# Optimization experiments

Measured on AMD Instinct MI355X. Metric: run time of the kernel, lower is better.

The kernel has to match this reference:

```python
import jax, jax.numpy as jnp
import numpy as np

D_MODEL, Q, V, H = 1024, 64, 64, 16
B, K = 2, 2048


def setup_inputs() -> dict:
    key = jax.random.key(0)
    ks = jax.random.split(key, 8)
    s = 0.02
    return {
        "xi": jax.random.normal(ks[0], (B, K, D_MODEL), dtype=jnp.float32),
        # stacked per-head projection weights (equivalent to h separate nn.Linear)
        "Wq": jax.random.normal(ks[1], (H, D_MODEL, Q), dtype=jnp.float32) * s,
        "bq": jax.random.normal(ks[2], (H, Q), dtype=jnp.float32) * s,
        "Wk": jax.random.normal(ks[3], (H, D_MODEL, Q), dtype=jnp.float32) * s,
        "bk": jax.random.normal(ks[4], (H, Q), dtype=jnp.float32) * s,
        "Wv": jax.random.normal(ks[5], (H, D_MODEL, V), dtype=jnp.float32) * s,
        "bv": jax.random.normal(ks[6], (H, V), dtype=jnp.float32) * s,
        "Wo": jax.random.normal(ks[7], (H * V, D_MODEL), dtype=jnp.float32) * s,
        "bo": jnp.zeros((D_MODEL,), dtype=jnp.float32),
    }


def reference(xi, Wq, bq, Wk, bk, Wv, bv, Wo, bo):
    # per-head projections, batched over heads: [B,H,K,q]
    queries = jnp.einsum("bkd,hdq->bhkq", xi, Wq) + bq[None, :, None, :]
    keys = jnp.einsum("bkd,hdq->bhkq", xi, Wk) + bk[None, :, None, :]
    values = jnp.einsum("bkd,hdv->bhkv", xi, Wv) + bv[None, :, None, :]
    # NOTE: original scales by sqrt(queries.shape[1]) == sqrt(seq_len K), not sqrt(q)
    scale = 1.0 / np.sqrt(xi.shape[1]).astype(np.float32)
    scores = jax.nn.softmax(jnp.einsum("bhkq,bhmq->bhkm", queries, keys) * scale, axis=-1)
    attn = jnp.einsum("bhkm,bhmv->bhkv", scores, values)  # [B,H,K,v]
    # concat heads along last dim -> [B,K,H*v]
    attn = attn.transpose(0, 2, 1, 3).reshape(xi.shape[0], xi.shape[1], -1)
    return attn @ Wo + bo
```

## Files before the change

### kernel.cpp

```cpp
#include <hip/hip_runtime.h>
#include <math.h>

typedef __bf16 bf16x8 __attribute__((ext_vector_type(8)));
typedef float  f32x4  __attribute__((ext_vector_type(4)));
typedef float  f32x16 __attribute__((ext_vector_type(16)));
typedef unsigned short u16x8 __attribute__((ext_vector_type(8)));

#define D_MODEL 1024
#define QDIM    64
#define HEADS   16
#define BATCH   2
#define SEQ     2048
#define M_ROWS  (BATCH*SEQ)
#define NCAT    (HEADS*3*QDIM)

__device__ __forceinline__ unsigned short f2bf(float f) {
    unsigned int u = __float_as_uint(f);
    u += 0x7fffu + ((u >> 16) & 1u);
    return (unsigned short)(u >> 16);
}

__device__ __forceinline__ void gl16(const unsigned short* g, unsigned short* l) {
    __builtin_amdgcn_global_load_lds(
        (const __attribute__((address_space(1))) unsigned int*)g,
        (__attribute__((address_space(3))) unsigned int*)l, 16, 0, 0);
}

__global__ __launch_bounds__(256) void k_cvt_bf16(const float* __restrict__ in,
                                                  unsigned short* __restrict__ out) {
    int i = (blockIdx.x * 256 + threadIdx.x) * 8;
    f32x4 a = *(const f32x4*)(in + i);
    f32x4 b = *(const f32x4*)(in + i + 4);
    u16x8 o;
    o[0]=f2bf(a[0]); o[1]=f2bf(a[1]); o[2]=f2bf(a[2]); o[3]=f2bf(a[3]);
    o[4]=f2bf(b[0]); o[5]=f2bf(b[1]); o[6]=f2bf(b[2]); o[7]=f2bf(b[3]);
    *(u16x8*)(out + i) = o;
}

__global__ __launch_bounds__(256) void k_prep_wcat(const float* __restrict__ Wq,
                                                   const float* __restrict__ Wk,
                                                   const float* __restrict__ Wv,
                                                   const float* __restrict__ bq,
                                                   const float* __restrict__ bk,
                                                   const float* __restrict__ bv,
                                                   unsigned short* __restrict__ WcatT,
                                                   float* __restrict__ bcat,
                                                   float qscale) {
    int blk = blockIdx.x;
    int dt = blk & 15, h = (blk >> 4) & 15, s = blk >> 8;
    const float* W = (s == 0) ? Wq : (s == 1) ? Wk : Wv;
    float sc = (s == 0) ? qscale : 1.0f;
    __shared__ float t[64][65];
    int tid = threadIdx.x;
    int dr = tid >> 2, qc = (tid & 3) * 16;
    const float* src = W + (size_t)h * (D_MODEL * QDIM) + (size_t)(dt * 64 + dr) * QDIM + qc;
#pragma unroll
    for (int j = 0; j < 4; ++j) {
        f32x4 v = *(const f32x4*)(src + j * 4);
        t[dr][qc + j * 4 + 0] = v[0]; t[dr][qc + j * 4 + 1] = v[1];
        t[dr][qc + j * 4 + 2] = v[2]; t[dr][qc + j * 4 + 3] = v[3];
    }
    __syncthreads();
    int q = tid >> 2, dc = (tid & 3) * 16;
    unsigned short* dst = WcatT + (size_t)(h * 192 + s * 64 + q) * D_MODEL + dt * 64 + dc;
#pragma unroll
    for (int j = 0; j < 2; ++j) {
        u16x8 o;
#pragma unroll
        for (int e = 0; e < 8; ++e) o[e] = f2bf(t[dc + j * 8 + e][q] * sc);
        *(u16x8*)(dst + j * 8) = o;
    }
    if (dt == 0 && tid < 64) {
        const float* bb = (s == 0) ? bq : (s == 1) ? bk : bv;
        bcat[h * 192 + s * 64 + tid] = bb[h * QDIM + tid] * sc;
    }
}

__global__ __launch_bounds__(256) void k_prep_wo(const float* __restrict__ Wo,
                                                 unsigned short* __restrict__ WoT) {
    int blk = blockIdx.x;
    int ct = blk & 15, rt = blk >> 4;
    __shared__ float t[64][65];
    int tid = threadIdx.x;
    int dr = tid >> 2, qc = (tid & 3) * 16;
    const float* src = Wo + (size_t)(rt * 64 + dr) * D_MODEL + ct * 64 + qc;
#pragma unroll
    for (int j = 0; j < 4; ++j) {
        f32x4 v = *(const f32x4*)(src + j * 4);
        t[dr][qc + j * 4 + 0] = v[0]; t[dr][qc + j * 4 + 1] = v[1];
        t[dr][qc + j * 4 + 2] = v[2]; t[dr][qc + j * 4 + 3] = v[3];
    }
    __syncthreads();
    int q = tid >> 2, dc = (tid & 3) * 16;
    unsigned short* dst = WoT + (size_t)(ct * 64 + q) * D_MODEL + rt * 64 + dc;
#pragma unroll
    for (int j = 0; j < 2; ++j) {
        u16x8 o;
#pragma unroll
        for (int e = 0; e < 8; ++e) o[e] = f2bf(t[dc + j * 8 + e][q]);
        *(u16x8*)(dst + j * 8) = o;
    }
}

template<bool OUT_BF16>
__global__ __launch_bounds__(256) void k_gemm(const unsigned short* __restrict__ A,
                                              const unsigned short* __restrict__ BT,
                                              const float* __restrict__ bias,
                                              void* __restrict__ Cout,
                                              int N, int Kd) {
    __shared__ __align__(16) unsigned char smem[65536];
    const int tid = threadIdx.x;
    const int lane = tid & 63, w = tid >> 6;
    const int g = lane >> 4, c = lane & 15;
    int nwg = gridDim.x * gridDim.y;
    int bid = blockIdx.y * gridDim.x + blockIdx.x;
    int sw = (bid & 7) * (nwg >> 3) + (bid >> 3);
    int bx = sw % gridDim.x, by = sw / gridDim.x;
    const int m0 = by * 128, n0 = bx * 128;
    const int wm = (w >> 1) * 64, wn = (w & 1) * 64;
    f32x4 acc[4][4] = {};

    const int srow = w * 16 + (lane >> 2);
    const int scol = ((lane & 3) ^ ((lane >> 3) & 3)) * 8;
    const unsigned short* pA0 = A  + (size_t)(m0 + srow) * Kd + scol;
    const unsigned short* pA1 = pA0 + (size_t)64 * Kd;
    const unsigned short* pB0 = BT + (size_t)(n0 + srow) * Kd + scol;
    const unsigned short* pB1 = pB0 + (size_t)64 * Kd;
    const int kc = (c >> 1) & 3;
    const int aoff = (wm + c) * 64 + ((g ^ kc) * 16);
    const int boff = (wn + c) * 64 + ((g ^ kc) * 16);

#define STAGE(buf)                                                                   \
    {                                                                                \
        unsigned short* lb = (unsigned short*)(smem + (buf) * 16384) + w * 512;      \
        gl16(pA0, lb);                                                               \
        gl16(pA1, lb + 2048);                                                        \
        gl16(pB0, lb + 4096);                                                        \
        gl16(pB1, lb + 6144);                                                        \
        pA0 += 32; pA1 += 32; pB0 += 32; pB1 += 32;                                  \
    }

#define COMPUTE(buf)                                                                 \
    {                                                                                \
        const unsigned char* Ab = smem + (buf) * 16384;                              \
        const unsigned char* Bb = Ab + 8192;                                         \
        bf16x8 af[4], bfr[4];                                                        \
        _Pragma("unroll") for (int mf = 0; mf < 4; ++mf)                             \
            af[mf] = *(const bf16x8*)(Ab + mf * 1024 + aoff);                        \
        _Pragma("unroll") for (int nf = 0; nf < 4; ++nf)                             \
            bfr[nf] = *(const bf16x8*)(Bb + nf * 1024 + boff);                       \
        __builtin_amdgcn_s_setprio(1);                                               \
        _Pragma("unroll") for (int mf = 0; mf < 4; ++mf)                             \
            _Pragma("unroll") for (int nf = 0; nf < 4; ++nf)                         \
                acc[mf][nf] = __builtin_amdgcn_mfma_f32_16x16x32_bf16(               \
                    af[mf], bfr[nf], acc[mf][nf], 0, 0, 0);                          \
        __builtin_amdgcn_s_setprio(0);                                               \
    }

    const int nt = Kd >> 5;
    STAGE(0); STAGE(1); STAGE(2);

    for (int t = 0; t < nt - 3; ++t) {
        STAGE((t + 3) & 3);
        asm volatile("s_waitcnt vmcnt(12)" ::: "memory");
        __builtin_amdgcn_s_barrier();
        __builtin_amdgcn_sched_barrier(0);
        COMPUTE(t & 3);
        __builtin_amdgcn_sched_barrier(0);
        __builtin_amdgcn_s_barrier();
    }
    asm volatile("s_waitcnt vmcnt(8)" ::: "memory");
    __builtin_amdgcn_s_barrier();
    __builtin_amdgcn_sched_barrier(0);
    COMPUTE((nt - 3) & 3);
    __builtin_amdgcn_sched_barrier(0);
    __builtin_amdgcn_s_barrier();
    asm volatile("s_waitcnt vmcnt(4)" ::: "memory");
    __builtin_amdgcn_s_barrier();
    __builtin_amdgcn_sched_barrier(0);
    COMPUTE((nt - 2) & 3);
    __builtin_amdgcn_sched_barrier(0);
    __builtin_amdgcn_s_barrier();
    asm volatile("s_waitcnt vmcnt(0)" ::: "memory");
    __builtin_amdgcn_s_barrier();
    __builtin_amdgcn_sched_barrier(0);
    COMPUTE((nt - 1) & 3);
#undef STAGE
#undef COMPUTE

#pragma unroll
    for (int mf = 0; mf < 4; ++mf)
#pragma unroll
        for (int nf = 0; nf < 4; ++nf) {
            int col = n0 + wn + nf * 16 + c;
            float bb = bias[col];
#pragma unroll
            for (int r = 0; r < 4; ++r) {
                int row = m0 + wm + mf * 16 + 4 * g + r;
                float v = acc[mf][nf][r] + bb;
                if (OUT_BF16)
                    ((unsigned short*)Cout)[(size_t)row * N + col] = f2bf(v);
                else
                    ((float*)Cout)[(size_t)row * N + col] = v;
            }
        }
}

__global__ __launch_bounds__(256) void k_repack(const unsigned short* __restrict__ qkv,
                                                unsigned short* __restrict__ kfrag,
                                                unsigned short* __restrict__ vfrag) {
    int blk = blockIdx.x;
    int kt = blk & 31, h = (blk >> 5) & 15, b = blk >> 9;
    __shared__ unsigned short ktile[64][72];
    __shared__ unsigned short vtile[64][72];
    int tid = threadIdx.x;
#pragma unroll
    for (int j = 0; j < 2; ++j) {
        int cid = tid + j * 256;
        int row = cid >> 3, ch = (cid & 7) * 8;
        const unsigned short* base = qkv + (size_t)(b * SEQ + kt * 64 + row) * NCAT + h * 192;
        *(u16x8*)&ktile[row][ch] = *(const u16x8*)(base + 64 + ch);
        *(u16x8*)&vtile[row][ch] = *(const u16x8*)(base + 128 + ch);
    }
    __syncthreads();
    size_t obase = (size_t)blk * 4096;
#pragma unroll
    for (int j = 0; j < 2; ++j) {
        int p = tid + j * 256;
        int f = p >> 6, l31 = p & 31, hi = (p >> 5) & 1;
        *(u16x8*)(kfrag + obase + p * 8) =
            *(const u16x8*)&ktile[(f >> 2) * 32 + l31][(f & 3) * 16 + hi * 8];
        int vv = (f & 1) * 32 + l31;
        int k0 = (f >> 2) * 32 + ((f >> 1) & 1) * 16 + hi * 8;
        u16x8 o;
#pragma unroll
        for (int e = 0; e < 8; ++e) o[e] = vtile[k0 + e][vv];
        *(u16x8*)(vfrag + obase + p * 8) = o;
    }
}

__global__ __launch_bounds__(256) void k_attn(const unsigned short* __restrict__ qkv,
                                              const unsigned short* __restrict__ kfrag,
                                              const unsigned short* __restrict__ vfrag,
                                              unsigned short* __restrict__ attn) {
    int bid = blockIdx.x;
    int blk = (bid & 7) * 128 + (bid >> 3);
    int qt = blk & 31, h = (blk >> 5) & 15, b = blk >> 9;
    int tid = threadIdx.x, w = tid >> 6, lane = tid & 63;
    int l31 = lane & 31, hi = lane >> 5;
    int qh = w & 1, kh = w >> 1;

    __shared__ __align__(16) unsigned char KV[2][16384];

    const int qbase = b * SEQ + qt * 64;
    const unsigned short* qrow = qkv + (size_t)(qbase + qh * 32 + l31) * NCAT + h * 192;
    bf16x8 qf[4];
#pragma unroll
    for (int s = 0; s < 4; ++s) qf[s] = *(const bf16x8*)(qrow + s * 16 + hi * 8);

    f32x16 o0 = {}, o1 = {};
    float rsum = 0.f;

    const size_t fb = (size_t)(b * 512 + h * 32) * 4096;
    const unsigned short* ks0 = kfrag + fb + (w)     * 512 + lane * 8;
    const unsigned short* ks1 = kfrag + fb + (w + 4) * 512 + lane * 8;
    const unsigned short* vs0 = vfrag + fb + (w)     * 512 + lane * 8;
    const unsigned short* vs1 = vfrag + fb + (w + 4) * 512 + lane * 8;
    const unsigned kd0 = w * 1024, kd1 = (w + 4) * 1024;
    const unsigned vd0 = 8192 + w * 1024, vd1 = 8192 + (w + 4) * 1024;
    const int lx = lane * 16;

    gl16(ks0, (unsigned short*)&KV[0][kd0]);
    gl16(vs0, (unsigned short*)&KV[0][vd0]);
    gl16(ks1, (unsigned short*)&KV[0][kd1]);
    gl16(vs1, (unsigned short*)&KV[0][vd1]);
    ks0 += 4096; ks1 += 4096; vs0 += 4096; vs1 += 4096;
    asm volatile("s_waitcnt vmcnt(0)" ::: "memory");
    __builtin_amdgcn_s_barrier();

    const int NT = SEQ / 64;
    for (int t = 0; t < NT; ++t) {
        const int cur = t & 1;
        if (t + 1 < NT) {
            gl16(ks0, (unsigned short*)&KV[cur ^ 1][kd0]);
            gl16(vs0, (unsigned short*)&KV[cur ^ 1][vd0]);
            gl16(ks1, (unsigned short*)&KV[cur ^ 1][kd1]);
            gl16(vs1, (unsigned short*)&KV[cur ^ 1][vd1]);
            ks0 += 4096; ks1 += 4096; vs0 += 4096; vs1 += 4096;
            asm volatile("s_waitcnt vmcnt(4)" ::: "memory");
        } else {
            asm volatile("s_waitcnt vmcnt(0)" ::: "memory");
        }
        __builtin_amdgcn_s_barrier();
        __builtin_amdgcn_sched_barrier(0);

        const unsigned char* Kf = &KV[cur][0];
        const unsigned char* Vf = &KV[cur][8192];

        f32x16 st = {};
        __builtin_amdgcn_s_setprio(1);
#pragma unroll
        for (int s = 0; s < 4; ++s) {
            bf16x8 kf = *(const bf16x8*)(Kf + (kh * 4 + s) * 1024 + lx);
            st = __builtin_amdgcn_mfma_f32_32x32x16_bf16(kf, qf[s], st, 0, 0, 0);
        }
        __builtin_amdgcn_s_setprio(0);

#pragma unroll
        for (int r = 0; r < 16; ++r) {
            float p = __builtin_amdgcn_exp2f(st[r]);
            st[r] = p;
            rsum += p;
        }
        unsigned int d0, d1, d2, d3, d4, d5, d6, d7;
        asm("v_cvt_pk_bf16_f32 %0, %1, %2" : "=v"(d0) : "v"(st[0]),  "v"(st[1]));
        asm("v_cvt_pk_bf16_f32 %0, %1, %2" : "=v"(d1) : "v"(st[2]),  "v"(st[3]));
        asm("v_cvt_pk_bf16_f32 %0, %1, %2" : "=v"(d2) : "v"(st[4]),  "v"(st[5]));
        asm("v_cvt_pk_bf16_f32 %0, %1, %2" : "=v"(d3) : "v"(st[6]),  "v"(st[7]));
        asm("v_cvt_pk_bf16_f32 %0, %1, %2" : "=v"(d4) : "v"(st[8]),  "v"(st[9]));
        asm("v_cvt_pk_bf16_f32 %0, %1, %2" : "=v"(d5) : "v"(st[10]), "v"(st[11]));
        asm("v_cvt_pk_bf16_f32 %0, %1, %2" : "=v"(d6) : "v"(st[12]), "v"(st[13]));
        asm("v_cvt_pk_bf16_f32 %0, %1, %2" : "=v"(d7) : "v"(st[14]), "v"(st[15]));
        asm("v_permlane32_swap_b32 %0, %1" : "+v"(d0), "+v"(d2));
        asm("v_permlane32_swap_b32 %0, %1" : "+v"(d1), "+v"(d3));
        asm("v_permlane32_swap_b32 %0, %1" : "+v"(d4), "+v"(d6));
        asm("v_permlane32_swap_b32 %0, %1" : "+v"(d5), "+v"(d7));
        union { unsigned int u[4]; bf16x8 v; } pa0, pa1;
        pa0.u[0] = d0; pa0.u[1] = d1; pa0.u[2] = d2; pa0.u[3] = d3;
        pa1.u[0] = d4; pa1.u[1] = d5; pa1.u[2] = d6; pa1.u[3] = d7;

        __builtin_amdgcn_s_setprio(1);
        {
            bf16x8 vf00 = *(const bf16x8*)(Vf + (kh * 4 + 0) * 1024 + lx);
            bf16x8 vf01 = *(const bf16x8*)(Vf + (kh * 4 + 1) * 1024 + lx);
            bf16x8 vf10 = *(const bf16x8*)(Vf + (kh * 4 + 2) * 1024 + lx);
            bf16x8 vf11 = *(const bf16x8*)(Vf + (kh * 4 + 3) * 1024 + lx);
            o0 = __builtin_amdgcn_mfma_f32_32x32x16_bf16(pa0.v, vf00, o0, 0, 0, 0);
            o1 = __builtin_amdgcn_mfma_f32_32x32x16_bf16(pa0.v, vf01, o1, 0, 0, 0);
            o0 = __builtin_amdgcn_mfma_f32_32x32x16_bf16(pa1.v, vf10, o0, 0, 0, 0);
            o1 = __builtin_amdgcn_mfma_f32_32x32x16_bf16(pa1.v, vf11, o1, 0, 0, 0);
        }
        __builtin_amdgcn_s_setprio(0);
        __builtin_amdgcn_sched_barrier(0);
        __builtin_amdgcn_s_barrier();
    }

    rsum += __shfl_xor(rsum, 32);
    __syncthreads();
    float* red = (float*)&KV[0][0];
    float* rsb = (float*)&KV[1][0];
    if (kh == 1) {
#pragma unroll
        for (int r = 0; r < 16; ++r) {
            int q = (r & 3) + 8 * (r >> 2) + 4 * hi;
            red[(qh * 32 + q) * 64 + l31]      = o0[r];
            red[(qh * 32 + q) * 64 + 32 + l31] = o1[r];
        }
    }
    if (lane < 32) rsb[(kh * 2 + qh) * 32 + l31] = rsum;
    __syncthreads();
    if (kh == 0) {
#pragma unroll
        for (int r = 0; r < 16; ++r) {
            int q = (r & 3) + 8 * (r >> 2) + 4 * hi;
            float tot = rsb[qh * 32 + q] + rsb[(2 + qh) * 32 + q];
            float inv = 1.0f / tot;
            float v0 = (o0[r] + red[(qh * 32 + q) * 64 + l31]) * inv;
            float v1 = (o1[r] + red[(qh * 32 + q) * 64 + 32 + l31]) * inv;
            int row = qbase + qh * 32 + q;
            attn[(size_t)row * (HEADS * QDIM) + h * QDIM + l31]      = f2bf(v0);
            attn[(size_t)row * (HEADS * QDIM) + h * QDIM + 32 + l31] = f2bf(v1);
        }
    }
}

extern "C" void kernel_launch(void* const* d_in, const int* in_sizes, int n_in,
                              void* d_out, int out_size, void* d_ws, size_t ws_size,
                              hipStream_t stream) {
    const float* xi = (const float*)d_in[0];
    const float* Wq = (const float*)d_in[1];
    const float* bq = (const float*)d_in[2];
    const float* Wk = (const float*)d_in[3];
    const float* bk = (const float*)d_in[4];
    const float* Wv = (const float*)d_in[5];
    const float* bv = (const float*)d_in[6];
    const float* Wo = (const float*)d_in[7];
    const float* bo = (const float*)d_in[8];

    unsigned short* xi_bf = (unsigned short*)d_ws;
    unsigned short* WcatT = xi_bf + (size_t)M_ROWS * D_MODEL;
    unsigned short* WoT   = WcatT + (size_t)NCAT * D_MODEL;
    float*          bcat  = (float*)(WoT + (size_t)D_MODEL * D_MODEL);
    unsigned short* qkvc  = (unsigned short*)(bcat + NCAT);
    unsigned short* kfrag = qkvc + (size_t)M_ROWS * NCAT;
    unsigned short* vfrag = kfrag + (size_t)BATCH * HEADS * 32 * 4096;
    unsigned short* attnb = vfrag + (size_t)BATCH * HEADS * 32 * 4096;

    float qscale = 1.4426950408889634f / sqrtf((float)SEQ);

    k_cvt_bf16<<<(M_ROWS * D_MODEL) / 2048, 256, 0, stream>>>(xi, xi_bf);
    k_prep_wcat<<<768, 256, 0, stream>>>(Wq, Wk, Wv, bq, bk, bv, WcatT, bcat, qscale);
    k_prep_wo<<<256, 256, 0, stream>>>(Wo, WoT);

    k_gemm<true><<<dim3(NCAT / 128, M_ROWS / 128), 256, 0, stream>>>(
        xi_bf, WcatT, bcat, (void*)qkvc, NCAT, D_MODEL);

    k_repack<<<BATCH * HEADS * (SEQ / 64), 256, 0, stream>>>(qkvc, kfrag, vfrag);

    k_attn<<<BATCH * HEADS * (SEQ / 64), 256, 0, stream>>>(qkvc, kfrag, vfrag, attnb);

    k_gemm<false><<<dim3(D_MODEL / 128, M_ROWS / 128), 256, 0, stream>>>(
        attnb, WoT, bo, d_out, D_MODEL, D_MODEL);
}
```

Measured before the change: 127.1 us.

## Load K/V fragments directly to registers in attention and merge weight-prep kernels

The attention kernel drops the LDS double buffer and its barriers. Each wave now loads only the K/V fragments it uses (its kh half) straight from global memory into registers, ping-ponging between two register sets so the next tile's loads overlap the current tile's compute. This removes per-tile block synchronisation and LDS round trips, at the cost of more VGPRs and of relying on L2 hits, since the two waves sharing a kh read the same data. Separately, the Wqkv and Wo weight-transpose kernels are fused into one launch to save a kernel launch.

Measured after the change: 119.6 us. -5.9%, faster.

```diff
diff --git a/kernel.cpp b/kernel.cpp
--- a/kernel.cpp
+++ b/kernel.cpp
@@ -37,68 +37,66 @@
     *(u16x8*)(out + i) = o;
 }
 
-__global__ __launch_bounds__(256) void k_prep_wcat(const float* __restrict__ Wq,
-                                                   const float* __restrict__ Wk,
-                                                   const float* __restrict__ Wv,
-                                                   const float* __restrict__ bq,
-                                                   const float* __restrict__ bk,
-                                                   const float* __restrict__ bv,
-                                                   unsigned short* __restrict__ WcatT,
-                                                   float* __restrict__ bcat,
-                                                   float qscale) {
-    int blk = blockIdx.x;
-    int dt = blk & 15, h = (blk >> 4) & 15, s = blk >> 8;
-    const float* W = (s == 0) ? Wq : (s == 1) ? Wk : Wv;
-    float sc = (s == 0) ? qscale : 1.0f;
+__global__ __launch_bounds__(256) void k_prep_w(const float* __restrict__ Wq,
+                                                const float* __restrict__ Wk,
+                                                const float* __restrict__ Wv,
+                                                const float* __restrict__ bq,
+                                                const float* __restrict__ bk,
+                                                const float* __restrict__ bv,
+                                                const float* __restrict__ Wo,
+                                                unsigned short* __restrict__ WcatT,
+                                                float* __restrict__ bcat,
+                                                unsigned short* __restrict__ WoT,
+                                                float qscale) {
     __shared__ float t[64][65];
     int tid = threadIdx.x;
     int dr = tid >> 2, qc = (tid & 3) * 16;
-    const float* src = W + (size_t)h * (D_MODEL * QDIM) + (size_t)(dt * 64 + dr) * QDIM + qc;
-#pragma unroll
-    for (int j = 0; j < 4; ++j) {
-        f32x4 v = *(const f32x4*)(src + j * 4);
-        t[dr][qc + j * 4 + 0] = v[0]; t[dr][qc + j * 4 + 1] = v[1];
-        t[dr][qc + j * 4 + 2] = v[2]; t[dr][qc + j * 4 + 3] = v[3];
-    }
-    __syncthreads();
-    int q = tid >> 2, dc = (tid & 3) * 16;
-    unsigned short* dst = WcatT + (size_t)(h * 192 + s * 64 + q) * D_MODEL + dt * 64 + dc;
-#pragma unroll
-    for (int j = 0; j < 2; ++j) {
-        u16x8 o;
-#pragma unroll
-        for (int e = 0; e < 8; ++e) o[e] = f2bf(t[dc + j * 8 + e][q] * sc);
-        *(u16x8*)(dst + j * 8) = o;
-    }
-    if (dt == 0 && tid < 64) {
-        const float* bb = (s == 0) ? bq : (s == 1) ? bk : bv;
-        bcat[h * 192 + s * 64 + tid] = bb[h * QDIM + tid] * sc;
-    }
-}
-
-__global__ __launch_bounds__(256) void k_prep_wo(const float* __restrict__ Wo,
-                                                 unsigned short* __restrict__ WoT) {
-    int blk = blockIdx.x;
-    int ct = blk & 15, rt = blk >> 4;
-    __shared__ float t[64][65];
-    int tid = threadIdx.x;
-    int dr = tid >> 2, qc = (tid & 3) * 16;
-    const float* src = Wo + (size_t)(rt * 64 + dr) * D_MODEL + ct * 64 + qc;
-#pragma unroll
-    for (int j = 0; j < 4; ++j) {
-        f32x4 v = *(const f32x4*)(src + j * 4);
-        t[dr][qc + j * 4 + 0] = v[0]; t[dr][qc + j * 4 + 1] = v[1];
-        t[dr][qc + j * 4 + 2] = v[2]; t[dr][qc + j * 4 + 3] = v[3];
-    }
-    __syncthreads();
-    int q = tid >> 2, dc = (tid & 3) * 16;
-    unsigned short* dst = WoT + (size_t)(ct * 64 + q) * D_MODEL + rt * 64 + dc;
-#pragma unroll
-    for (int j = 0; j < 2; ++j) {
-        u16x8 o;
-#pragma unroll
-        for (int e = 0; e < 8; ++e) o[e] = f2bf(t[dc + j * 8 + e][q]);
-        *(u16x8*)(dst + j * 8) = o;
+    if (blockIdx.x < 768) {
+        int blk = blockIdx.x;
+        int dt = blk & 15, h = (blk >> 4) & 15, s = blk >> 8;
+        const float* W = (s == 0) ? Wq : (s == 1) ? Wk : Wv;
+        float sc = (s == 0) ? qscale : 1.0f;
+        const float* src = W + (size_t)h * (D_MODEL * QDIM) + (size_t)(dt * 64 + dr) * QDIM + qc;
+#pragma unroll
+        for (int j = 0; j < 4; ++j) {
+            f32x4 v = *(const f32x4*)(src + j * 4);
+            t[dr][qc + j * 4 + 0] = v[0]; t[dr][qc + j * 4 + 1] = v[1];
+            t[dr][qc + j * 4 + 2] = v[2]; t[dr][qc + j * 4 + 3] = v[3];
+        }
+        __syncthreads();
+        int q = tid >> 2, dc = (tid & 3) * 16;
+        unsigned short* dst = WcatT + (size_t)(h * 192 + s * 64 + q) * D_MODEL + dt * 64 + dc;
+#pragma unroll
+        for (int j = 0; j < 2; ++j) {
+            u16x8 o;
+#pragma unroll
+            for (int e = 0; e < 8; ++e) o[e] = f2bf(t[dc + j * 8 + e][q] * sc);
+            *(u16x8*)(dst + j * 8) = o;
+        }
+        if (dt == 0 && tid < 64) {
+            const float* bb = (s == 0) ? bq : (s == 1) ? bk : bv;
+            bcat[h * 192 + s * 64 + tid] = bb[h * QDIM + tid] * sc;
+        }
+    } else {
+        int blk = blockIdx.x - 768;
+        int ct = blk & 15, rt = blk >> 4;
+        const float* src = Wo + (size_t)(rt * 64 + dr) * D_MODEL + ct * 64 + qc;
+#pragma unroll
+        for (int j = 0; j < 4; ++j) {
+            f32x4 v = *(const f32x4*)(src + j * 4);
+            t[dr][qc + j * 4 + 0] = v[0]; t[dr][qc + j * 4 + 1] = v[1];
+            t[dr][qc + j * 4 + 2] = v[2]; t[dr][qc + j * 4 + 3] = v[3];
+        }
+        __syncthreads();
+        int q = tid >> 2, dc = (tid & 3) * 16;
+        unsigned short* dst = WoT + (size_t)(ct * 64 + q) * D_MODEL + rt * 64 + dc;
+#pragma unroll
+        for (int j = 0; j < 2; ++j) {
+            u16x8 o;
+#pragma unroll
+            for (int e = 0; e < 8; ++e) o[e] = f2bf(t[dc + j * 8 + e][q]);
+            *(u16x8*)(dst + j * 8) = o;
+        }
     }
 }
 
@@ -250,105 +248,87 @@
     int l31 = lane & 31, hi = lane >> 5;
     int qh = w & 1, kh = w >> 1;
 
-    __shared__ __align__(16) unsigned char KV[2][16384];
+    __shared__ float red[4096];
+    __shared__ float rsb[128];
 
     const int qbase = b * SEQ + qt * 64;
     const unsigned short* qrow = qkv + (size_t)(qbase + qh * 32 + l31) * NCAT + h * 192;
-    bf16x8 qf[4];
-#pragma unroll
-    for (int s = 0; s < 4; ++s) qf[s] = *(const bf16x8*)(qrow + s * 16 + hi * 8);
+    bf16x8 qf0 = *(const bf16x8*)(qrow + 0 * 16 + hi * 8);
+    bf16x8 qf1 = *(const bf16x8*)(qrow + 1 * 16 + hi * 8);
+    bf16x8 qf2 = *(const bf16x8*)(qrow + 2 * 16 + hi * 8);
+    bf16x8 qf3 = *(const bf16x8*)(qrow + 3 * 16 + hi * 8);
 
     f32x16 o0 = {}, o1 = {};
     float rsum = 0.f;
 
-    const size_t fb = (size_t)(b * 512 + h * 32) * 4096;
-    const unsigned short* ks0 = kfrag + fb + (w)     * 512 + lane * 8;
-    const unsigned short* ks1 = kfrag + fb + (w + 4) * 512 + lane * 8;
-    const unsigned short* vs0 = vfrag + fb + (w)     * 512 + lane * 8;
-    const unsigned short* vs1 = vfrag + fb + (w + 4) * 512 + lane * 8;
-    const unsigned kd0 = w * 1024, kd1 = (w + 4) * 1024;
-    const unsigned vd0 = 8192 + w * 1024, vd1 = 8192 + (w + 4) * 1024;
-    const int lx = lane * 16;
-
-    gl16(ks0, (unsigned short*)&KV[0][kd0]);
-    gl16(vs0, (unsigned short*)&KV[0][vd0]);
-    gl16(ks1, (unsigned short*)&KV[0][kd1]);
-    gl16(vs1, (unsigned short*)&KV[0][vd1]);
-    ks0 += 4096; ks1 += 4096; vs0 += 4096; vs1 += 4096;
-    asm volatile("s_waitcnt vmcnt(0)" ::: "memory");
-    __builtin_amdgcn_s_barrier();
+    const size_t fb = (size_t)(b * 512 + h * 32) * 4096 + (size_t)(kh * 4) * 512 + lane * 8;
+    const unsigned short* kp = kfrag + fb;
+    const unsigned short* vp = vfrag + fb;
+
+    bf16x8 aK0, aK1, aK2, aK3, aV0, aV1, aV2, aV3;
+    bf16x8 bK0, bK1, bK2, bK3, bV0, bV1, bV2, bV3;
+
+#define LOADT(K0, K1, K2, K3, V0, V1, V2, V3)                   \
+    {                                                           \
+        K0 = *(const bf16x8*)(kp);                              \
+        K1 = *(const bf16x8*)(kp + 512);                        \
+        K2 = *(const bf16x8*)(kp + 1024);                       \
+        K3 = *(const bf16x8*)(kp + 1536);                       \
+        V0 = *(const bf16x8*)(vp);                              \
+        V1 = *(const bf16x8*)(vp + 512);                        \
+        V2 = *(const bf16x8*)(vp + 1024);                       \
+        V3 = *(const bf16x8*)(vp + 1536);                       \
+        kp += 4096; vp += 4096;                                 \
+    }
+
+#define COMPUTE(K0, K1, K2, K3, V0, V1, V2, V3)                                       \
+    {                                                                                 \
+        f32x16 st = {};                                                               \
+        st = __builtin_amdgcn_mfma_f32_32x32x16_bf16(K0, qf0, st, 0, 0, 0);           \
+        st = __builtin_amdgcn_mfma_f32_32x32x16_bf16(K1, qf1, st, 0, 0, 0);           \
+        st = __builtin_amdgcn_mfma_f32_32x32x16_bf16(K2, qf2, st, 0, 0, 0);           \
+        st = __builtin_amdgcn_mfma_f32_32x32x16_bf16(K3, qf3, st, 0, 0, 0);           \
+        _Pragma("unroll") for (int r = 0; r < 16; ++r) {                              \
+            float p = __builtin_amdgcn_exp2f(st[r]);                                  \
+            st[r] = p;                                                                \
+            rsum += p;                                                                \
+        }                                                                             \
+        unsigned int d0, d1, d2, d3, d4, d5, d6, d7;                                  \
+        asm("v_cvt_pk_bf16_f32 %0, %1, %2" : "=v"(d0) : "v"(st[0]),  "v"(st[1]));     \
+        asm("v_cvt_pk_bf16_f32 %0, %1, %2" : "=v"(d1) : "v"(st[2]),  "v"(st[3]));     \
+        asm("v_cvt_pk_bf16_f32 %0, %1, %2" : "=v"(d2) : "v"(st[4]),  "v"(st[5]));     \
+        asm("v_cvt_pk_bf16_f32 %0, %1, %2" : "=v"(d3) : "v"(st[6]),  "v"(st[7]));     \
+        asm("v_cvt_pk_bf16_f32 %0, %1, %2" : "=v"(d4) : "v"(st[8]),  "v"(st[9]));     \
+        asm("v_cvt_pk_bf16_f32 %0, %1, %2" : "=v"(d5) : "v"(st[10]), "v"(st[11]));    \
+        asm("v_cvt_pk_bf16_f32 %0, %1, %2" : "=v"(d6) : "v"(st[12]), "v"(st[13]));    \
+        asm("v_cvt_pk_bf16_f32 %0, %1, %2" : "=v"(d7) : "v"(st[14]), "v"(st[15]));    \
+        asm("v_permlane32_swap_b32 %0, %1" : "+v"(d0), "+v"(d2));                     \
+        asm("v_permlane32_swap_b32 %0, %1" : "+v"(d1), "+v"(d3));                     \
+        asm("v_permlane32_swap_b32 %0, %1" : "+v"(d4), "+v"(d6));                     \
+        asm("v_permlane32_swap_b32 %0, %1" : "+v"(d5), "+v"(d7));                     \
+        union { unsigned int u[4]; bf16x8 v; } pa0, pa1;                              \
+        pa0.u[0] = d0; pa0.u[1] = d1; pa0.u[2] = d2; pa0.u[3] = d3;                   \
+        pa1.u[0] = d4; pa1.u[1] = d5; pa1.u[2] = d6; pa1.u[3] = d7;                   \
+        o0 = __builtin_amdgcn_mfma_f32_32x32x16_bf16(pa0.v, V0, o0, 0, 0, 0);         \
+        o1 = __builtin_amdgcn_mfma_f32_32x32x16_bf16(pa0.v, V1, o1, 0, 0, 0);         \
+        o0 = __builtin_amdgcn_mfma_f32_32x32x16_bf16(pa1.v, V2, o0, 0, 0, 0);         \
+        o1 = __builtin_amdgcn_mfma_f32_32x32x16_bf16(pa1.v, V3, o1, 0, 0, 0);         \
+    }
+
+    LOADT(aK0, aK1, aK2, aK3, aV0, aV1, aV2, aV3);
 
     const int NT = SEQ / 64;
-    for (int t = 0; t < NT; ++t) {
-        const int cur = t & 1;
-        if (t + 1 < NT) {
-            gl16(ks0, (unsigned short*)&KV[cur ^ 1][kd0]);
-            gl16(vs0, (unsigned short*)&KV[cur ^ 1][vd0]);
-            gl16(ks1, (unsigned short*)&KV[cur ^ 1][kd1]);
-            gl16(vs1, (unsigned short*)&KV[cur ^ 1][vd1]);
-            ks0 += 4096; ks1 += 4096; vs0 += 4096; vs1 += 4096;
-            asm volatile("s_waitcnt vmcnt(4)" ::: "memory");
-        } else {
-            asm volatile("s_waitcnt vmcnt(0)" ::: "memory");
-        }
-        __builtin_amdgcn_s_barrier();
-        __builtin_amdgcn_sched_barrier(0);
-
-        const unsigned char* Kf = &KV[cur][0];
-        const unsigned char* Vf = &KV[cur][8192];
-
-        f32x16 st = {};
-        __builtin_amdgcn_s_setprio(1);
-#pragma unroll
-        for (int s = 0; s < 4; ++s) {
-            bf16x8 kf = *(const bf16x8*)(Kf + (kh * 4 + s) * 1024 + lx);
-            st = __builtin_amdgcn_mfma_f32_32x32x16_bf16(kf, qf[s], st, 0, 0, 0);
-        }
-        __builtin_amdgcn_s_setprio(0);
-
-#pragma unroll
-        for (int r = 0; r < 16; ++r) {
-            float p = __builtin_amdgcn_exp2f(st[r]);
-            st[r] = p;
-            rsum += p;
-        }
-        unsigned int d0, d1, d2, d3, d4, d5, d6, d7;
-        asm("v_cvt_pk_bf16_f32 %0, %1, %2" : "=v"(d0) : "v"(st[0]),  "v"(st[1]));
-        asm("v_cvt_pk_bf16_f32 %0, %1, %2" : "=v"(d1) : "v"(st[2]),  "v"(st[3]));
-        asm("v_cvt_pk_bf16_f32 %0, %1, %2" : "=v"(d2) : "v"(st[4]),  "v"(st[5]));
-        asm("v_cvt_pk_bf16_f32 %0, %1, %2" : "=v"(d3) : "v"(st[6]),  "v"(st[7]));
-        asm("v_cvt_pk_bf16_f32 %0, %1, %2" : "=v"(d4) : "v"(st[8]),  "v"(st[9]));
-        asm("v_cvt_pk_bf16_f32 %0, %1, %2" : "=v"(d5) : "v"(st[10]), "v"(st[11]));
-        asm("v_cvt_pk_bf16_f32 %0, %1, %2" : "=v"(d6) : "v"(st[12]), "v"(st[13]));
-        asm("v_cvt_pk_bf16_f32 %0, %1, %2" : "=v"(d7) : "v"(st[14]), "v"(st[15]));
-        asm("v_permlane32_swap_b32 %0, %1" : "+v"(d0), "+v"(d2));
-        asm("v_permlane32_swap_b32 %0, %1" : "+v"(d1), "+v"(d3));
-        asm("v_permlane32_swap_b32 %0, %1" : "+v"(d4), "+v"(d6));
-        asm("v_permlane32_swap_b32 %0, %1" : "+v"(d5), "+v"(d7));
-        union { unsigned int u[4]; bf16x8 v; } pa0, pa1;
-        pa0.u[0] = d0; pa0.u[1] = d1; pa0.u[2] = d2; pa0.u[3] = d3;
-        pa1.u[0] = d4; pa1.u[1] = d5; pa1.u[2] = d6; pa1.u[3] = d7;
-
-        __builtin_amdgcn_s_setprio(1);
-        {
-            bf16x8 vf00 = *(const bf16x8*)(Vf + (kh * 4 + 0) * 1024 + lx);
-            bf16x8 vf01 = *(const bf16x8*)(Vf + (kh * 4 + 1) * 1024 + lx);
-            bf16x8 vf10 = *(const bf16x8*)(Vf + (kh * 4 + 2) * 1024 + lx);
-            bf16x8 vf11 = *(const bf16x8*)(Vf + (kh * 4 + 3) * 1024 + lx);
-            o0 = __builtin_amdgcn_mfma_f32_32x32x16_bf16(pa0.v, vf00, o0, 0, 0, 0);
-            o1 = __builtin_amdgcn_mfma_f32_32x32x16_bf16(pa0.v, vf01, o1, 0, 0, 0);
-            o0 = __builtin_amdgcn_mfma_f32_32x32x16_bf16(pa1.v, vf10, o0, 0, 0, 0);
-            o1 = __builtin_amdgcn_mfma_f32_32x32x16_bf16(pa1.v, vf11, o1, 0, 0, 0);
-        }
-        __builtin_amdgcn_s_setprio(0);
-        __builtin_amdgcn_sched_barrier(0);
-        __builtin_amdgcn_s_barrier();
-    }
+    for (int t = 0; t < NT; t += 2) {
+        LOADT(bK0, bK1, bK2, bK3, bV0, bV1, bV2, bV3);
+        COMPUTE(aK0, aK1, aK2, aK3, aV0, aV1, aV2, aV3);
+        if (t + 2 < NT)
+            LOADT(aK0, aK1, aK2, aK3, aV0, aV1, aV2, aV3);
+        COMPUTE(bK0, bK1, bK2, bK3, bV0, bV1, bV2, bV3);
+    }
+#undef LOADT
+#undef COMPUTE
 
     rsum += __shfl_xor(rsum, 32);
-    __syncthreads();
-    float* red = (float*)&KV[0][0];
-    float* rsb = (float*)&KV[1][0];
     if (kh == 1) {
 #pragma unroll
         for (int r = 0; r < 16; ++r) {
@@ -399,8 +379,7 @@
     float qscale = 1.4426950408889634f / sqrtf((float)SEQ);
 
     k_cvt_bf16<<<(M_ROWS * D_MODEL) / 2048, 256, 0, stream>>>(xi, xi_bf);
-    k_prep_wcat<<<768, 256, 0, stream>>>(Wq, Wk, Wv, bq, bk, bv, WcatT, bcat, qscale);
-    k_prep_wo<<<256, 256, 0, stream>>>(Wo, WoT);
+    k_prep_w<<<1024, 256, 0, stream>>>(Wq, Wk, Wv, bq, bk, bv, Wo, WcatT, bcat, WoT, qscale);
 
     k_gemm<true><<<dim3(NCAT / 128, M_ROWS / 128), 256, 0, stream>>>(
         xi_bf, WcatT, bcat, (void*)qkvc, NCAT, D_MODEL);
```
